# Kernel optimization log

Measured on AMD Instinct MI355X. Metric: run time of the kernel, lower is better.

## Reference

```python
import jax, jax.numpy as jnp
import numpy as np

NUM_LAYERS, E, H = 4, 256, 8
HD = E // H
EPS = 1e-5


def _layer_norm(x, g, b):
    m = jnp.mean(x, axis=-1, keepdims=True)
    v = jnp.mean((x - m) ** 2, axis=-1, keepdims=True)
    return (x - m) / jnp.sqrt(v + EPS) * g + b


def _embed_rotary(x, pos):
    # x: [B, L, E], pos: [B, L, E, 2] (cos, sin)
    x2 = jnp.stack([-x[..., 1::2], x[..., ::2]], axis=-1).reshape(x.shape)
    return x * pos[..., 0] + x2 * pos[..., 1]


def setup_inputs() -> dict:
    key = jax.random.key(0)
    ks = jax.random.split(key, 16)
    Lq, B, Lkv = 512, 4, 4096
    s = 0.02
    return {
        "query": jax.random.normal(ks[0], (Lq, B, E), jnp.float32),
        "value": jax.random.normal(ks[1], (Lkv, B, E), jnp.float32),
        "query_pos": jax.random.normal(ks[2], (B, Lq, E, 2), jnp.float32),
        "value_pos": jax.random.normal(ks[3], (B, Lkv, E, 2), jnp.float32),
        "Wqkv": jax.random.normal(ks[4], (NUM_LAYERS, 3 * E, E), jnp.float32) * s,
        "bqkv": jnp.zeros((NUM_LAYERS, 3 * E), jnp.float32),
        "Wo": jax.random.normal(ks[5], (NUM_LAYERS, E, E), jnp.float32) * s,
        "bo": jnp.zeros((NUM_LAYERS, E), jnp.float32),
        "ln1_g": jnp.ones((NUM_LAYERS, E), jnp.float32),
        "ln1_b": jnp.zeros((NUM_LAYERS, E), jnp.float32),
        "W1": jax.random.normal(ks[6], (NUM_LAYERS, E, E), jnp.float32) * s,
        "b1": jnp.zeros((NUM_LAYERS, E), jnp.float32),
        "W2": jax.random.normal(ks[7], (NUM_LAYERS, E, E), jnp.float32) * s,
        "b2": jnp.zeros((NUM_LAYERS, E), jnp.float32),
        "ln2_g": jnp.ones((NUM_LAYERS, E), jnp.float32),
        "ln2_b": jnp.zeros((NUM_LAYERS, E), jnp.float32),
    }


def reference(query, value, query_pos, value_pos, Wqkv, bqkv, Wo, bo,
              ln1_g, ln1_b, W1, b1, W2, b2, ln2_g, ln2_b):
    Lq, B, _ = query.shape
    Lkv = value.shape[0]
    scale = HD ** -0.5

    def step(q_in, p):
        Wqkv_l, bqkv_l, Wo_l, bo_l, g1, be1, W1_l, b1_l, W2_l, b2_l, g2, be2 = p
        Wq, Wk, Wv = jnp.split(Wqkv_l, 3, axis=0)
        bq, bk, bv = jnp.split(bqkv_l, 3, axis=0)
        q = (q_in @ Wq.T + bq) * scale              # [Lq, B, E] (scaled as torch MHA)
        k = value @ Wk.T + bk                        # [Lkv, B, E]
        v = value @ Wv.T + bv
        qb = _embed_rotary(q.swapaxes(0, 1), query_pos)   # [B, Lq, E]
        kb = _embed_rotary(k.swapaxes(0, 1), value_pos)   # [B, Lkv, E]
        vb = v.swapaxes(0, 1)
        qh = qb.reshape(B, Lq, H, HD).transpose(0, 2, 1, 3)    # [B, H, Lq, HD]
        kh = kb.reshape(B, Lkv, H, HD).transpose(0, 2, 1, 3)
        vh = vb.reshape(B, Lkv, H, HD).transpose(0, 2, 1, 3)
        attn = jax.nn.softmax(jnp.einsum('bhqd,bhkd->bhqk', qh, kh), axis=-1)
        o = jnp.einsum('bhqk,bhkd->bhqd', attn, vh)            # [B, H, Lq, HD]
        o = o.transpose(0, 2, 1, 3).reshape(B, Lq, E).swapaxes(0, 1)  # [Lq, B, E]
        x = _layer_norm(q_in + o @ Wo_l.T + bo_l, g1, be1)
        ff = jax.nn.relu(x @ W1_l.T + b1_l) @ W2_l.T + b2_l
        y = _layer_norm(x + ff, g2, be2)
        return y, y

    params = (Wqkv, bqkv, Wo, bo, ln1_g, ln1_b, W1, b1, W2, b2, ln2_g, ln2_b)
    _, ys = jax.lax.scan(step, query, params)
    return ys  # [num_layers, Lq, B, E] — stacked per-layer outputs
```

## Files before the change

### kernel.cpp

```cpp
#include <hip/hip_runtime.h>
#include <hip/hip_bf16.h>

typedef __attribute__((ext_vector_type(8))) short short8;
typedef __attribute__((ext_vector_type(4))) float float4v;

#define LQ 512
#define NB 4
#define LKV 4096
#define E 256
#define NH 8
#define HD 32
#define NLAYER 4
#define QSCALE 0.17677669529663687f
#define SPLITS 8
#define KSPAN (LKV / SPLITS)
#define QT 128
#define CK 128

#define LDS_FENCE() asm volatile("s_waitcnt lgkmcnt(0)" ::: "memory")

__device__ __forceinline__ unsigned short f2bf(float f) {
    union { float f; unsigned int i; } x; x.f = f;
    unsigned int r = x.i + 0x7fffu + ((x.i >> 16) & 1u);
    return (unsigned short)(r >> 16);
}
__device__ __forceinline__ unsigned int pack2(float a, float b) {
    union { float f; unsigned int i; } xa, xb; xa.f = a; xb.f = b;
    unsigned int ra = xa.i + 0x7fffu + ((xa.i >> 16) & 1u);
    unsigned int rb = xb.i + 0x7fffu + ((xb.i >> 16) & 1u);
    return (ra >> 16) | (rb & 0xffff0000u);
}
__device__ __forceinline__ unsigned int pack2_rtz(float a, float b) {
    union { float f; unsigned int i; } xa, xb; xa.f = a; xb.f = b;
    return __builtin_amdgcn_perm(xb.i, xa.i, 0x07060302u);
}
__device__ __forceinline__ float bf2f(unsigned short u) {
    union { unsigned int i; float f; } x; x.i = ((unsigned int)u) << 16; return x.f;
}
__device__ __forceinline__ float4v mfma16(short8 a, short8 b, float4v c) {
    return __builtin_amdgcn_mfma_f32_16x16x32_bf16(a, b, c, 0, 0, 0);
}
__device__ __forceinline__ void pack_store8(const float* __restrict__ src,
                                            unsigned short* __restrict__ dst) {
    float4 a = *(const float4*)src;
    float4 b = *(const float4*)(src + 4);
    uint4 v;
    v.x = pack2(a.x, a.y); v.y = pack2(a.z, a.w);
    v.z = pack2(b.x, b.y); v.w = pack2(b.z, b.w);
    *(uint4*)dst = v;
}

__global__ void pack_all(const float* __restrict__ value, const float* __restrict__ Wqkv,
                         const float* __restrict__ Wo, const float* __restrict__ W1,
                         const float* __restrict__ W2, const float* __restrict__ qpos,
                         const float* __restrict__ vpos, const float* __restrict__ query,
                         unsigned short* __restrict__ val_t, unsigned short* __restrict__ wqkv_bf,
                         unsigned short* __restrict__ wo_bf, unsigned short* __restrict__ w1_bf,
                         unsigned short* __restrict__ w2_bf, unsigned short* __restrict__ qpos_bf,
                         unsigned short* __restrict__ vpos_bf, float* __restrict__ cur,
                         unsigned short* __restrict__ cur_bf) {
    int bid = blockIdx.x;
    if (bid < 2048) {
        long idx = ((long)bid * 256 + threadIdx.x) * 8;
        int ro = (int)(idx >> 8), e = (int)(idx & 255);
        int ri = ((ro & 4095) << 2) | (ro >> 12);
        pack_store8(value + (long)ri * 256 + e, val_t + idx);
        return;
    }
    bid -= 2048;
    if (bid < 384) { long i = ((long)bid * 256 + threadIdx.x) * 8; pack_store8(Wqkv + i, wqkv_bf + i); return; }
    bid -= 384;
    if (bid < 128) { long i = ((long)bid * 256 + threadIdx.x) * 8; pack_store8(Wo + i, wo_bf + i); return; }
    bid -= 128;
    if (bid < 128) { long i = ((long)bid * 256 + threadIdx.x) * 8; pack_store8(W1 + i, w1_bf + i); return; }
    bid -= 128;
    if (bid < 128) { long i = ((long)bid * 256 + threadIdx.x) * 8; pack_store8(W2 + i, w2_bf + i); return; }
    bid -= 128;
    if (bid < 512) { long i = ((long)bid * 256 + threadIdx.x) * 8; pack_store8(qpos + i, qpos_bf + i); return; }
    bid -= 512;
    if (bid < 4096) { long i = ((long)bid * 256 + threadIdx.x) * 8; pack_store8(vpos + i, vpos_bf + i); return; }
    bid -= 4096;
    {
        long i = ((long)bid * 256 + threadIdx.x) * 8;
        float4 a = *(const float4*)&query[i];
        float4 b = *(const float4*)&query[i + 4];
        *(float4*)&cur[i] = a;
        *(float4*)&cur[i + 4] = b;
        uint4 v;
        v.x = pack2(a.x, a.y); v.y = pack2(a.z, a.w);
        v.z = pack2(b.x, b.y); v.w = pack2(b.z, b.w);
        *(uint4*)&cur_bf[i] = v;
    }
}

__global__ __launch_bounds__(256) void gemm_k(
        const unsigned short* __restrict__ A, const unsigned short* __restrict__ W,
        const float* __restrict__ bias, unsigned short* __restrict__ out_bf) {
    __shared__ unsigned short sA[32 * 264];
    __shared__ unsigned short sB[64 * 264];
    const int t = threadIdx.x;
    const int lane = t & 63, wave = t >> 6, quad = lane >> 4, lid = lane & 15;
    const int row0 = blockIdx.x * 32, col0 = blockIdx.y * 64;
    {
        int r = t >> 3, ks = (t & 7) * 32;
        const unsigned short* ap = A + (long)(row0 + r) * E + ks;
#pragma unroll
        for (int i = 0; i < 4; i++)
            *(uint4*)&sA[r * 264 + ks + i * 8] = *(const uint4*)(ap + i * 8);
    }
    {
        int r = t >> 2, ks = (t & 3) * 64;
        const unsigned short* wp = W + (long)(col0 + r) * E + ks;
#pragma unroll
        for (int i = 0; i < 8; i++)
            *(uint4*)&sB[r * 264 + ks + i * 8] = *(const uint4*)(wp + i * 8);
    }
    __syncthreads();
    float4v acc[2];
    acc[0] = (float4v){0.f, 0.f, 0.f, 0.f};
    acc[1] = (float4v){0.f, 0.f, 0.f, 0.f};
#pragma unroll
    for (int k0 = 0; k0 < E; k0 += 32) {
        short8 bf = *(const short8*)&sB[(wave * 16 + lid) * 264 + k0 + quad * 8];
        short8 af0 = *(const short8*)&sA[(lid) * 264 + k0 + quad * 8];
        short8 af1 = *(const short8*)&sA[(16 + lid) * 264 + k0 + quad * 8];
        acc[0] = mfma16(af0, bf, acc[0]);
        acc[1] = mfma16(af1, bf, acc[1]);
    }
#pragma unroll
    for (int mt = 0; mt < 2; mt++)
#pragma unroll
        for (int r = 0; r < 4; r++) {
            int grow = row0 + mt * 16 + quad * 4 + r;
            int gcol = col0 + wave * 16 + lid;
            float v = fmaxf(acc[mt][r] + bias[gcol], 0.f);
            out_bf[(long)grow * E + gcol] = f2bf(v);
        }
}

template <int COMBINE, int OUT2>
__global__ __launch_bounds__(256, 1) void gemm_ln(
        const unsigned short* __restrict__ A,
        const float* __restrict__ Opart, const float* __restrict__ lp,
        const unsigned short* __restrict__ W, const float* __restrict__ bias,
        const float* __restrict__ res, const float* __restrict__ g,
        const float* __restrict__ bvec, float* __restrict__ outf,
        unsigned short* __restrict__ out_bf, float* __restrict__ outf2) {
    __shared__ unsigned short sA[16 * 264];
    __shared__ float lnS[4][16];
    __shared__ float lnQ[4][16];
    const int t = threadIdx.x;
    const int lane = t & 63, wave = t >> 6, quad = lane >> 4, lid = lane & 15;
    const int row0 = blockIdx.x * 16;
    {
        const int r = t >> 4, cseg = t & 15;
        if (COMBINE) {
            const int grow = row0 + r;
            const int seq = grow >> 2, b = grow & 3;
            const int h = cseg >> 1, dd = (cseg & 1) * 16;
            const int bh = b * 8 + h;
            float L = 0.f;
            float av[16];
#pragma unroll
            for (int j = 0; j < 16; j++) av[j] = 0.f;
#pragma unroll
            for (int s = 0; s < SPLITS; s++) {
                long rbase = (long)(s * 32 + bh) * 512 + seq;
                L += lp[rbase];
#pragma unroll
                for (int jj = 0; jj < 4; jj++) {
                    float4 p = *(const float4*)&Opart[rbase * 32 + dd + jj * 4];
                    av[jj * 4 + 0] += p.x; av[jj * 4 + 1] += p.y;
                    av[jj * 4 + 2] += p.z; av[jj * 4 + 3] += p.w;
                }
            }
            float inv = 1.f / L;
            uint4 u0, u1;
            u0.x = pack2(av[0] * inv, av[1] * inv);   u0.y = pack2(av[2] * inv, av[3] * inv);
            u0.z = pack2(av[4] * inv, av[5] * inv);   u0.w = pack2(av[6] * inv, av[7] * inv);
            u1.x = pack2(av[8] * inv, av[9] * inv);   u1.y = pack2(av[10] * inv, av[11] * inv);
            u1.z = pack2(av[12] * inv, av[13] * inv); u1.w = pack2(av[14] * inv, av[15] * inv);
            *(uint4*)&sA[r * 264 + cseg * 16] = u0;
            *(uint4*)&sA[r * 264 + cseg * 16 + 8] = u1;
        } else {
            const unsigned short* ap = A + (long)(row0 + r) * E + cseg * 16;
            *(uint4*)&sA[r * 264 + cseg * 16] = *(const uint4*)ap;
            *(uint4*)&sA[r * 264 + cseg * 16 + 8] = *(const uint4*)(ap + 8);
        }
    }
    __syncthreads();
    float4v acc[4];
#pragma unroll
    for (int nf = 0; nf < 4; nf++) acc[nf] = (float4v){0.f, 0.f, 0.f, 0.f};
#pragma unroll
    for (int k0 = 0; k0 < E; k0 += 32) {
        short8 af = *(const short8*)&sA[lid * 264 + k0 + quad * 8];
#pragma unroll
        for (int nf = 0; nf < 4; nf++) {
            short8 bf = *(const short8*)(W + (long)(wave * 64 + nf * 16 + lid) * E + k0 + quad * 8);
            acc[nf] = mfma16(af, bf, acc[nf]);
        }
    }
    float v[4][4];
    float sr[4], qr_[4];
#pragma unroll
    for (int r = 0; r < 4; r++) { sr[r] = 0.f; qr_[r] = 0.f; }
#pragma unroll
    for (int nf = 0; nf < 4; nf++) {
        int col = wave * 64 + nf * 16 + lid;
        float bcol = bias[col];
#pragma unroll
        for (int r = 0; r < 4; r++) {
            int grow = row0 + quad * 4 + r;
            float val = acc[nf][r] + bcol + res[(long)grow * E + col];
            v[nf][r] = val;
            sr[r] += val;
            qr_[r] += val * val;
        }
    }
#pragma unroll
    for (int r = 0; r < 4; r++) {
#pragma unroll
        for (int d = 1; d < 16; d <<= 1) {
            sr[r] += __shfl_xor(sr[r], d);
            qr_[r] += __shfl_xor(qr_[r], d);
        }
    }
    if (lid == 0) {
#pragma unroll
        for (int r = 0; r < 4; r++) {
            lnS[wave][quad * 4 + r] = sr[r];
            lnQ[wave][quad * 4 + r] = qr_[r];
        }
    }
    __syncthreads();
    float mean[4], rstd[4];
#pragma unroll
    for (int r = 0; r < 4; r++) {
        int row = quad * 4 + r;
        float S = lnS[0][row] + lnS[1][row] + lnS[2][row] + lnS[3][row];
        float Q = lnQ[0][row] + lnQ[1][row] + lnQ[2][row] + lnQ[3][row];
        float mu = S * (1.f / 256.f);
        float var = Q * (1.f / 256.f) - mu * mu;
        mean[r] = mu;
        rstd[r] = rsqrtf(var + 1e-5f);
    }
#pragma unroll
    for (int nf = 0; nf < 4; nf++) {
        int col = wave * 64 + nf * 16 + lid;
        float gc = g[col], bc = bvec[col];
#pragma unroll
        for (int r = 0; r < 4; r++) {
            int grow = row0 + quad * 4 + r;
            float xo = (v[nf][r] - mean[r]) * rstd[r] * gc + bc;
            outf[(long)grow * E + col] = xo;
            out_bf[(long)grow * E + col] = f2bf(xo);
            if (OUT2) outf2[(long)grow * E + col] = xo;
        }
    }
}

__global__ __launch_bounds__(256) void qkv_q(
        const unsigned short* __restrict__ A, const unsigned short* __restrict__ W,
        const float* __restrict__ bias, const unsigned short* __restrict__ pos,
        unsigned short* __restrict__ qout) {
    __shared__ unsigned short sA[32 * 40];
    __shared__ unsigned short sB[64 * 40];
    const int t = threadIdx.x;
    const int lane = t & 63, wave = t >> 6, quad = lane >> 4, lid = lane & 15;
    const int row0 = blockIdx.x * 32, col0 = blockIdx.y * 64;
    const int sr = t >> 2, sk = (t & 3) * 8;
    const unsigned short* ap = A + (long)(row0 + sr) * E + sk;
    const unsigned short* wp = W + (long)(col0 + sr) * E + sk;
    uint4 av, bv;
    if (t < 128) av = *(const uint4*)ap;
    bv = *(const uint4*)wp;
    float4v acc[2];
    acc[0] = (float4v){0.f, 0.f, 0.f, 0.f};
    acc[1] = (float4v){0.f, 0.f, 0.f, 0.f};
#pragma unroll
    for (int ki = 0; ki < 8; ki++) {
        __syncthreads();
        if (t < 128) *(uint4*)&sA[sr * 40 + sk] = av;
        *(uint4*)&sB[sr * 40 + sk] = bv;
        __syncthreads();
        if (ki < 7) {
            if (t < 128) av = *(const uint4*)(ap + (ki + 1) * 32);
            bv = *(const uint4*)(wp + (ki + 1) * 32);
        }
        short8 af0 = *(const short8*)&sA[lid * 40 + quad * 8];
        short8 af1 = *(const short8*)&sA[(16 + lid) * 40 + quad * 8];
        short8 bf = *(const short8*)&sB[(wave * 16 + lid) * 40 + quad * 8];
        acc[0] = mfma16(af0, bf, acc[0]);
        acc[1] = mfma16(af1, bf, acc[1]);
    }
#pragma unroll
    for (int mt = 0; mt < 2; mt++)
#pragma unroll
        for (int r = 0; r < 4; r++) {
            int grow = row0 + mt * 16 + quad * 4 + r;
            int gcol = col0 + wave * 16 + lid;
            float v = (acc[mt][r] + bias[gcol]) * QSCALE;
            int seq = grow >> 2, b = grow & 3;
            int c = gcol;
            unsigned int cs = *(const unsigned int*)&pos[(((long)b * LQ + seq) * E + c) * 2];
            float cv = bf2f((unsigned short)cs), sv = bf2f((unsigned short)(cs >> 16));
            float p = __shfl_xor(v, 1);
            float x2 = (c & 1) ? p : -p;
            float rv = v * cv + x2 * sv;
            qout[(((long)b * NH + (c >> 5)) * LQ + seq) * HD + (c & 31)] = f2bf(rv);
        }
}

__global__ __launch_bounds__(256) void qkv_kv(
        const unsigned short* __restrict__ A, const unsigned short* __restrict__ Wall,
        const float* __restrict__ ball, const unsigned short* __restrict__ pos,
        unsigned short* __restrict__ kall, unsigned short* __restrict__ vtall) {
    const int layer = blockIdx.z;
    const unsigned short* W = Wall + (long)layer * 768 * 256 + 256 * 256;
    const float* bias = ball + (long)layer * 768 + 256;
    unsigned short* kout = kall + (long)layer * 4194304;
    unsigned short* vtout = vtall + (long)layer * 4194304;
    __shared__ unsigned short sA[64 * 72];
    __shared__ unsigned short sB[64 * 72];
    __shared__ unsigned short sT[64 * 72];
    const int t = threadIdx.x;
    const int lane = t & 63, wave = t >> 6, quad = lane >> 4, lid = lane & 15;
    const int wr = wave >> 1, wc = wave & 1;
    const int row0 = blockIdx.x * 64, col0 = blockIdx.y * 64;
    const int b = row0 >> 12, seq0 = row0 & 4095;
    const int r = t >> 2, kk = (t & 3) * 16;
    const unsigned short* apg = A + (long)(row0 + r) * E + kk;
    const unsigned short* wpg = W + (long)(col0 + r) * E + kk;
    uint4 a0 = *(const uint4*)apg,        a1 = *(const uint4*)(apg + 8);
    uint4 b0 = *(const uint4*)wpg,        b1 = *(const uint4*)(wpg + 8);
    float4v acc[2][2];
    for (int i = 0; i < 2; i++) for (int j = 0; j < 2; j++) acc[i][j] = (float4v){0.f, 0.f, 0.f, 0.f};
#pragma unroll
    for (int ki = 0; ki < 4; ki++) {
        __syncthreads();
        *(uint4*)&sA[r * 72 + kk] = a0; *(uint4*)&sA[r * 72 + kk + 8] = a1;
        *(uint4*)&sB[r * 72 + kk] = b0; *(uint4*)&sB[r * 72 + kk + 8] = b1;
        __syncthreads();
        if (ki < 3) {
            a0 = *(const uint4*)(apg + (ki + 1) * 64); a1 = *(const uint4*)(apg + (ki + 1) * 64 + 8);
            b0 = *(const uint4*)(wpg + (ki + 1) * 64); b1 = *(const uint4*)(wpg + (ki + 1) * 64 + 8);
        }
#pragma unroll
        for (int kf = 0; kf < 2; kf++) {
            const int ko = kf * 32 + quad * 8;
            short8 af0 = *(const short8*)&sA[(wr * 32 + lid) * 72 + ko];
            short8 af1 = *(const short8*)&sA[(wr * 32 + 16 + lid) * 72 + ko];
            short8 bf0 = *(const short8*)&sB[(wc * 32 + lid) * 72 + ko];
            short8 bf1 = *(const short8*)&sB[(wc * 32 + 16 + lid) * 72 + ko];
            acc[0][0] = mfma16(af0, bf0, acc[0][0]);
            acc[0][1] = mfma16(af0, bf1, acc[0][1]);
            acc[1][0] = mfma16(af1, bf0, acc[1][0]);
            acc[1][1] = mfma16(af1, bf1, acc[1][1]);
        }
    }
    if (col0 < 256) {
#pragma unroll
        for (int mt = 0; mt < 2; mt++)
#pragma unroll
            for (int nt = 0; nt < 2; nt++)
#pragma unroll
                for (int rr = 0; rr < 4; rr++) {
                    int m = wr * 32 + mt * 16 + quad * 4 + rr;
                    int c = col0 + wc * 32 + nt * 16 + lid;
                    int seq = seq0 + m;
                    float v = acc[mt][nt][rr] + bias[c];
                    unsigned int cs = *(const unsigned int*)&pos[(((long)b * LKV + seq) * E + c) * 2];
                    float cv = bf2f((unsigned short)cs), sv = bf2f((unsigned short)(cs >> 16));
                    float p = __shfl_xor(v, 1);
                    float x2 = (c & 1) ? p : -p;
                    float rv = v * cv + x2 * sv;
                    kout[(((long)b * NH + (c >> 5)) * LKV + seq) * HD + (c & 31)] = f2bf(rv);
                }
    } else {
#pragma unroll
        for (int mt = 0; mt < 2; mt++)
#pragma unroll
            for (int nt = 0; nt < 2; nt++) {
                int cl = wc * 32 + nt * 16 + lid;
                int so = wr * 32 + mt * 16 + quad * 4;
                float bcol = bias[col0 + cl];
                uint2 pw;
                pw.x = pack2(acc[mt][nt][0] + bcol, acc[mt][nt][1] + bcol);
                pw.y = pack2(acc[mt][nt][2] + bcol, acc[mt][nt][3] + bcol);
                *(uint2*)&sT[cl * 72 + so] = pw;
            }
        __syncthreads();
        const int cl = t >> 2, sc = (t & 3) * 16;
        uint4 u0 = *(const uint4*)&sT[cl * 72 + sc];
        uint4 u1 = *(const uint4*)&sT[cl * 72 + sc + 8];
        int cg = (col0 - 256) + cl;
        unsigned short* dst = vtout + (((long)b * NH + (cg >> 5)) * HD + (cg & 31)) * (long)LKV + seq0 + sc;
        *(uint4*)dst = u0;
        *(uint4*)(dst + 8) = u1;
    }
}

__global__ __launch_bounds__(256) void attn_k(
        const unsigned short* __restrict__ qb, const unsigned short* __restrict__ kb,
        const unsigned short* __restrict__ vtb, float* __restrict__ Opart,
        float* __restrict__ lpart) {
    __shared__ unsigned short sK[CK * 40];
    __shared__ unsigned short sVT[32 * 136];
    __shared__ unsigned short sPT[4 * 64 * 36];
    const int t = threadIdx.x;
    const int lane = t & 63, wave = t >> 6, quad = lane >> 4, lid = lane & 15;
    const int qt0 = blockIdx.x * QT;
    const int bh = blockIdx.y;
    const int key0 = blockIdx.z * KSPAN;
    const unsigned short* kbase = kb + (long)bh * LKV * HD;
    const unsigned short* vbase = vtb + (long)bh * HD * LKV;
    short8 aq[2];
#pragma unroll
    for (int mf = 0; mf < 2; mf++)
        aq[mf] = *(const short8*)(qb + ((long)bh * LQ + qt0 + wave * 32 + mf * 16 + lid) * HD + quad * 8);
    float4v o[2][2];
#pragma unroll
    for (int i = 0; i < 2; i++) for (int j = 0; j < 2; j++) o[i][j] = (float4v){0.f, 0.f, 0.f, 0.f};
    float l[8] = {0.f, 0.f, 0.f, 0.f, 0.f, 0.f, 0.f, 0.f};
    const int krow = t >> 1, khalf = (t & 1) * 16;
    const int vrow = t >> 3, vkoff = (t & 7) * 16;
    unsigned short* myPT = &sPT[wave * 64 * 36];
    uint4 kv0 = *(const uint4*)(kbase + (long)(key0 + krow) * HD + khalf);
    uint4 kv1 = *(const uint4*)(kbase + (long)(key0 + krow) * HD + khalf + 8);
    uint4 vv0 = *(const uint4*)(vbase + (long)vrow * LKV + key0 + vkoff);
    uint4 vv1 = *(const uint4*)(vbase + (long)vrow * LKV + key0 + vkoff + 8);
    for (int ck = key0; ck < key0 + KSPAN; ck += CK) {
        __syncthreads();
        *(uint4*)&sK[krow * 40 + khalf] = kv0;
        *(uint4*)&sK[krow * 40 + khalf + 8] = kv1;
        *(uint4*)&sVT[vrow * 136 + vkoff] = vv0;
        *(uint4*)&sVT[vrow * 136 + vkoff + 8] = vv1;
        __syncthreads();
        if (ck + CK < key0 + KSPAN) {
            kv0 = *(const uint4*)(kbase + (long)(ck + CK + krow) * HD + khalf);
            kv1 = *(const uint4*)(kbase + (long)(ck + CK + krow) * HD + khalf + 8);
            vv0 = *(const uint4*)(vbase + (long)vrow * LKV + ck + CK + vkoff);
            vv1 = *(const uint4*)(vbase + (long)vrow * LKV + ck + CK + vkoff + 8);
        }
#pragma unroll
        for (int half = 0; half < 2; half++) {
#pragma unroll
            for (int nf = 0; nf < 4; nf++) {
                short8 bk = *(const short8*)&sK[(half * 64 + nf * 16 + lid) * 40 + quad * 8];
#pragma unroll
                for (int mf = 0; mf < 2; mf++) {
                    float4v z = (float4v){0.f, 0.f, 0.f, 0.f};
                    float4v s = mfma16(aq[mf], bk, z);
                    float e0 = __expf(s[0]), e1 = __expf(s[1]);
                    float e2 = __expf(s[2]), e3 = __expf(s[3]);
                    l[mf * 4 + 0] += e0; l[mf * 4 + 1] += e1;
                    l[mf * 4 + 2] += e2; l[mf * 4 + 3] += e3;
                    uint2 pk;
                    pk.x = pack2_rtz(e0, e1);
                    pk.y = pack2_rtz(e2, e3);
                    *(uint2*)&myPT[(nf * 16 + lid) * 36 + mf * 16 + quad * 4] = pk;
                }
            }
            LDS_FENCE();
#pragma unroll
            for (int kb2 = 0; kb2 < 2; kb2++) {
                short8 bv0 = *(const short8*)&sVT[lid * 136 + half * 64 + kb2 * 32 + quad * 8];
                short8 bv1 = *(const short8*)&sVT[(16 + lid) * 136 + half * 64 + kb2 * 32 + quad * 8];
#pragma unroll
                for (int mf = 0; mf < 2; mf++) {
                    short8 ap;
#pragma unroll
                    for (int j = 0; j < 8; j++)
                        ap[j] = (short)myPT[(kb2 * 32 + quad * 8 + j) * 36 + mf * 16 + lid];
                    o[mf][0] = mfma16(ap, bv0, o[mf][0]);
                    o[mf][1] = mfma16(ap, bv1, o[mf][1]);
                }
            }
            LDS_FENCE();
        }
    }
#pragma unroll
    for (int i = 0; i < 8; i++) {
#pragma unroll
        for (int d = 1; d < 16; d <<= 1) l[i] += __shfl_xor(l[i], d);
    }
#pragma unroll
    for (int mf = 0; mf < 2; mf++)
#pragma unroll
        for (int r = 0; r < 4; r++) {
            long orow = ((long)blockIdx.z * 32 + bh) * LQ + qt0 + wave * 32 + mf * 16 + quad * 4 + r;
            Opart[orow * HD + lid] = o[mf][0][r];
            Opart[orow * HD + 16 + lid] = o[mf][1][r];
            if (lid == 0) lpart[orow] = l[mf * 4 + r];
        }
}

extern "C" void kernel_launch(void* const* d_in, const int* in_sizes, int n_in,
                              void* d_out, int out_size, void* d_ws, size_t ws_size,
                              hipStream_t stream) {
    (void)in_sizes; (void)n_in; (void)out_size; (void)ws_size;
    const float* query = (const float*)d_in[0];
    const float* value = (const float*)d_in[1];
    const float* qpos  = (const float*)d_in[2];
    const float* vpos  = (const float*)d_in[3];
    const float* Wqkv  = (const float*)d_in[4];
    const float* bqkv  = (const float*)d_in[5];
    const float* Wo    = (const float*)d_in[6];
    const float* bo    = (const float*)d_in[7];
    const float* g1    = (const float*)d_in[8];
    const float* be1   = (const float*)d_in[9];
    const float* W1    = (const float*)d_in[10];
    const float* b1    = (const float*)d_in[11];
    const float* W2    = (const float*)d_in[12];
    const float* b2    = (const float*)d_in[13];
    const float* g2    = (const float*)d_in[14];
    const float* be2   = (const float*)d_in[15];
    float* outp = (float*)d_out;

    char* w = (char*)d_ws;
    float*          cur     = (float*)(w + 0);
    unsigned short* cur_bf  = (unsigned short*)(w + (2l  << 20));
    unsigned short* qbuf    = (unsigned short*)(w + (3l  << 20));
    float*          xb      = (float*)(w + (4l  << 20));
    unsigned short* xb_bf   = (unsigned short*)(w + (6l  << 20));
    unsigned short* h1b_bf  = (unsigned short*)(w + (7l  << 20));
    float*          lp      = (float*)(w + (8l  << 20));
    float*          Opart   = (float*)(w + (9l  << 20));
    unsigned short* val_t   = (unsigned short*)(w + (25l << 20));
    unsigned short* wqkv_bf = (unsigned short*)(w + (33l << 20));
    unsigned short* wo_bf   = (unsigned short*)(w + (35l << 20));
    unsigned short* w1_bf   = (unsigned short*)(w + (36l << 20));
    unsigned short* w2_bf   = (unsigned short*)(w + (37l << 20));
    unsigned short* qpos_bf = (unsigned short*)(w + (38l << 20));
    unsigned short* vpos_bf = (unsigned short*)(w + (40l << 20));
    unsigned short* kbuf    = (unsigned short*)(w + (56l << 20));
    unsigned short* vtb     = (unsigned short*)(w + (88l << 20));

    pack_all<<<7680, 256, 0, stream>>>(value, Wqkv, Wo, W1, W2, qpos, vpos, query,
                                       val_t, wqkv_bf, wo_bf, w1_bf, w2_bf, qpos_bf,
                                       vpos_bf, cur, cur_bf);

    qkv_kv<<<dim3(256, 8, NLAYER), 256, 0, stream>>>(val_t, wqkv_bf, bqkv, vpos_bf, kbuf, vtb);

    for (int layer = 0; layer < NLAYER; layer++) {
        const unsigned short* Wl = wqkv_bf + (long)layer * 768 * 256;
        const float* bl = bqkv + (long)layer * 768;
        qkv_q<<<dim3(64, 4), 256, 0, stream>>>(cur_bf, Wl, bl, qpos_bf, qbuf);
        attn_k<<<dim3(LQ / QT, 32, SPLITS), 256, 0, stream>>>(
            qbuf, kbuf + (long)layer * 4194304, vtb + (long)layer * 4194304, Opart, lp);
        gemm_ln<1, 0><<<128, 256, 0, stream>>>(
            nullptr, Opart, lp, wo_bf + layer * 65536, bo + layer * 256,
            cur, g1 + layer * 256, be1 + layer * 256, xb, xb_bf, nullptr);
        gemm_k<<<dim3(64, 4), 256, 0, stream>>>(xb_bf, w1_bf + layer * 65536, b1 + layer * 256, h1b_bf);
        gemm_ln<0, 1><<<128, 256, 0, stream>>>(
            h1b_bf, nullptr, nullptr, w2_bf + layer * 65536, b2 + layer * 256,
            xb, g2 + layer * 256, be2 + layer * 256, cur, cur_bf,
            outp + (long)layer * LQ * NB * E);
    }
}
```

Baseline: 379.4 us.

## Keep attention probabilities in registers via shuffles and fuse FFN into one kernel

The attention kernel now computes S transposed (K as the A operand), so exponentiated scores can be rearranged into the PV MFMA operand layout with cross-lane shuffles. This removes the LDS round-trip and fences for the P tile, and the row-sum reduction shrinks to two xor shuffles. The FFN's two GEMMs are fused into one kernel that keeps the ReLU hidden activations in LDS, which drops one launch per layer and the global h1 buffer. The qkv_kv kernel also reuses one LDS region for the transpose buffer, lowering its shared memory use. In exchange, the FFN kernel runs only 128 blocks, each doing both GEMMs serially, and attention adds many shuffle instructions.

```diff
diff --git a/kernel.cpp b/kernel.cpp
--- a/kernel.cpp
+++ b/kernel.cpp
@@ -16,8 +16,6 @@
 #define KSPAN (LKV / SPLITS)
 #define QT 128
 #define CK 128
-
-#define LDS_FENCE() asm volatile("s_waitcnt lgkmcnt(0)" ::: "memory")
 
 __device__ __forceinline__ unsigned short f2bf(float f) {
     union { float f; unsigned int i; } x; x.f = f;
@@ -93,59 +91,12 @@
     }
 }
 
-__global__ __launch_bounds__(256) void gemm_k(
-        const unsigned short* __restrict__ A, const unsigned short* __restrict__ W,
-        const float* __restrict__ bias, unsigned short* __restrict__ out_bf) {
-    __shared__ unsigned short sA[32 * 264];
-    __shared__ unsigned short sB[64 * 264];
-    const int t = threadIdx.x;
-    const int lane = t & 63, wave = t >> 6, quad = lane >> 4, lid = lane & 15;
-    const int row0 = blockIdx.x * 32, col0 = blockIdx.y * 64;
-    {
-        int r = t >> 3, ks = (t & 7) * 32;
-        const unsigned short* ap = A + (long)(row0 + r) * E + ks;
-#pragma unroll
-        for (int i = 0; i < 4; i++)
-            *(uint4*)&sA[r * 264 + ks + i * 8] = *(const uint4*)(ap + i * 8);
-    }
-    {
-        int r = t >> 2, ks = (t & 3) * 64;
-        const unsigned short* wp = W + (long)(col0 + r) * E + ks;
-#pragma unroll
-        for (int i = 0; i < 8; i++)
-            *(uint4*)&sB[r * 264 + ks + i * 8] = *(const uint4*)(wp + i * 8);
-    }
-    __syncthreads();
-    float4v acc[2];
-    acc[0] = (float4v){0.f, 0.f, 0.f, 0.f};
-    acc[1] = (float4v){0.f, 0.f, 0.f, 0.f};
-#pragma unroll
-    for (int k0 = 0; k0 < E; k0 += 32) {
-        short8 bf = *(const short8*)&sB[(wave * 16 + lid) * 264 + k0 + quad * 8];
-        short8 af0 = *(const short8*)&sA[(lid) * 264 + k0 + quad * 8];
-        short8 af1 = *(const short8*)&sA[(16 + lid) * 264 + k0 + quad * 8];
-        acc[0] = mfma16(af0, bf, acc[0]);
-        acc[1] = mfma16(af1, bf, acc[1]);
-    }
-#pragma unroll
-    for (int mt = 0; mt < 2; mt++)
-#pragma unroll
-        for (int r = 0; r < 4; r++) {
-            int grow = row0 + mt * 16 + quad * 4 + r;
-            int gcol = col0 + wave * 16 + lid;
-            float v = fmaxf(acc[mt][r] + bias[gcol], 0.f);
-            out_bf[(long)grow * E + gcol] = f2bf(v);
-        }
-}
-
-template <int COMBINE, int OUT2>
-__global__ __launch_bounds__(256, 1) void gemm_ln(
-        const unsigned short* __restrict__ A,
+__global__ __launch_bounds__(256, 1) void wo_ln(
         const float* __restrict__ Opart, const float* __restrict__ lp,
         const unsigned short* __restrict__ W, const float* __restrict__ bias,
         const float* __restrict__ res, const float* __restrict__ g,
         const float* __restrict__ bvec, float* __restrict__ outf,
-        unsigned short* __restrict__ out_bf, float* __restrict__ outf2) {
+        unsigned short* __restrict__ out_bf) {
     __shared__ unsigned short sA[16 * 264];
     __shared__ float lnS[4][16];
     __shared__ float lnQ[4][16];
@@ -154,39 +105,33 @@
     const int row0 = blockIdx.x * 16;
     {
         const int r = t >> 4, cseg = t & 15;
-        if (COMBINE) {
-            const int grow = row0 + r;
-            const int seq = grow >> 2, b = grow & 3;
-            const int h = cseg >> 1, dd = (cseg & 1) * 16;
-            const int bh = b * 8 + h;
-            float L = 0.f;
-            float av[16];
-#pragma unroll
-            for (int j = 0; j < 16; j++) av[j] = 0.f;
-#pragma unroll
-            for (int s = 0; s < SPLITS; s++) {
-                long rbase = (long)(s * 32 + bh) * 512 + seq;
-                L += lp[rbase];
-#pragma unroll
-                for (int jj = 0; jj < 4; jj++) {
-                    float4 p = *(const float4*)&Opart[rbase * 32 + dd + jj * 4];
-                    av[jj * 4 + 0] += p.x; av[jj * 4 + 1] += p.y;
-                    av[jj * 4 + 2] += p.z; av[jj * 4 + 3] += p.w;
-                }
+        const int grow = row0 + r;
+        const int seq = grow >> 2, b = grow & 3;
+        const int h = cseg >> 1, dd = (cseg & 1) * 16;
+        const int bh = b * 8 + h;
+        float L = 0.f;
+        float av[16];
+#pragma unroll
+        for (int j = 0; j < 16; j++) av[j] = 0.f;
+#pragma unroll
+        for (int s = 0; s < SPLITS; s++) {
+            long rbase = (long)(s * 32 + bh) * 512 + seq;
+            L += lp[rbase];
+#pragma unroll
+            for (int jj = 0; jj < 4; jj++) {
+                float4 p = *(const float4*)&Opart[rbase * 32 + dd + jj * 4];
+                av[jj * 4 + 0] += p.x; av[jj * 4 + 1] += p.y;
+                av[jj * 4 + 2] += p.z; av[jj * 4 + 3] += p.w;
             }
-            float inv = 1.f / L;
-            uint4 u0, u1;
-            u0.x = pack2(av[0] * inv, av[1] * inv);   u0.y = pack2(av[2] * inv, av[3] * inv);
-            u0.z = pack2(av[4] * inv, av[5] * inv);   u0.w = pack2(av[6] * inv, av[7] * inv);
-            u1.x = pack2(av[8] * inv, av[9] * inv);   u1.y = pack2(av[10] * inv, av[11] * inv);
-            u1.z = pack2(av[12] * inv, av[13] * inv); u1.w = pack2(av[14] * inv, av[15] * inv);
-            *(uint4*)&sA[r * 264 + cseg * 16] = u0;
-            *(uint4*)&sA[r * 264 + cseg * 16 + 8] = u1;
-        } else {
-            const unsigned short* ap = A + (long)(row0 + r) * E + cseg * 16;
-            *(uint4*)&sA[r * 264 + cseg * 16] = *(const uint4*)ap;
-            *(uint4*)&sA[r * 264 + cseg * 16 + 8] = *(const uint4*)(ap + 8);
-        }
+        }
+        float inv = 1.f / L;
+        uint4 u0, u1;
+        u0.x = pack2(av[0] * inv, av[1] * inv);   u0.y = pack2(av[2] * inv, av[3] * inv);
+        u0.z = pack2(av[4] * inv, av[5] * inv);   u0.w = pack2(av[6] * inv, av[7] * inv);
+        u1.x = pack2(av[8] * inv, av[9] * inv);   u1.y = pack2(av[10] * inv, av[11] * inv);
+        u1.z = pack2(av[12] * inv, av[13] * inv); u1.w = pack2(av[14] * inv, av[15] * inv);
+        *(uint4*)&sA[r * 264 + cseg * 16] = u0;
+        *(uint4*)&sA[r * 264 + cseg * 16 + 8] = u1;
     }
     __syncthreads();
     float4v acc[4];
@@ -241,9 +186,8 @@
         float S = lnS[0][row] + lnS[1][row] + lnS[2][row] + lnS[3][row];
         float Q = lnQ[0][row] + lnQ[1][row] + lnQ[2][row] + lnQ[3][row];
         float mu = S * (1.f / 256.f);
-        float var = Q * (1.f / 256.f) - mu * mu;
         mean[r] = mu;
-        rstd[r] = rsqrtf(var + 1e-5f);
+        rstd[r] = rsqrtf(Q * (1.f / 256.f) - mu * mu + 1e-5f);
     }
 #pragma unroll
     for (int nf = 0; nf < 4; nf++) {
@@ -255,7 +199,117 @@
             float xo = (v[nf][r] - mean[r]) * rstd[r] * gc + bc;
             outf[(long)grow * E + col] = xo;
             out_bf[(long)grow * E + col] = f2bf(xo);
-            if (OUT2) outf2[(long)grow * E + col] = xo;
+        }
+    }
+}
+
+__global__ __launch_bounds__(256, 1) void ffn_ln(
+        const unsigned short* __restrict__ A, const unsigned short* __restrict__ W1,
+        const float* __restrict__ b1, const unsigned short* __restrict__ W2,
+        const float* __restrict__ b2, const float* __restrict__ res,
+        const float* __restrict__ g, const float* __restrict__ bvec,
+        float* __restrict__ outf, unsigned short* __restrict__ out_bf,
+        float* __restrict__ outf2) {
+    __shared__ unsigned short sA[16 * 264];
+    __shared__ unsigned short sH[16 * 264];
+    __shared__ float lnS[4][16];
+    __shared__ float lnQ[4][16];
+    const int t = threadIdx.x;
+    const int lane = t & 63, wave = t >> 6, quad = lane >> 4, lid = lane & 15;
+    const int row0 = blockIdx.x * 16;
+    {
+        const int r = t >> 4, cseg = t & 15;
+        const unsigned short* ap = A + (long)(row0 + r) * E + cseg * 16;
+        *(uint4*)&sA[r * 264 + cseg * 16] = *(const uint4*)ap;
+        *(uint4*)&sA[r * 264 + cseg * 16 + 8] = *(const uint4*)(ap + 8);
+    }
+    __syncthreads();
+    float4v acc[4];
+#pragma unroll
+    for (int nf = 0; nf < 4; nf++) acc[nf] = (float4v){0.f, 0.f, 0.f, 0.f};
+#pragma unroll
+    for (int k0 = 0; k0 < E; k0 += 32) {
+        short8 af = *(const short8*)&sA[lid * 264 + k0 + quad * 8];
+#pragma unroll
+        for (int nf = 0; nf < 4; nf++) {
+            short8 bf = *(const short8*)(W1 + (long)(wave * 64 + nf * 16 + lid) * E + k0 + quad * 8);
+            acc[nf] = mfma16(af, bf, acc[nf]);
+        }
+    }
+#pragma unroll
+    for (int nf = 0; nf < 4; nf++) {
+        int col = wave * 64 + nf * 16 + lid;
+        float bc = b1[col];
+#pragma unroll
+        for (int r = 0; r < 4; r++)
+            sH[(quad * 4 + r) * 264 + col] = f2bf(fmaxf(acc[nf][r] + bc, 0.f));
+    }
+    __syncthreads();
+#pragma unroll
+    for (int nf = 0; nf < 4; nf++) acc[nf] = (float4v){0.f, 0.f, 0.f, 0.f};
+#pragma unroll
+    for (int k0 = 0; k0 < E; k0 += 32) {
+        short8 af = *(const short8*)&sH[lid * 264 + k0 + quad * 8];
+#pragma unroll
+        for (int nf = 0; nf < 4; nf++) {
+            short8 bf = *(const short8*)(W2 + (long)(wave * 64 + nf * 16 + lid) * E + k0 + quad * 8);
+            acc[nf] = mfma16(af, bf, acc[nf]);
+        }
+    }
+    float v[4][4];
+    float sr[4], qr_[4];
+#pragma unroll
+    for (int r = 0; r < 4; r++) { sr[r] = 0.f; qr_[r] = 0.f; }
+#pragma unroll
+    for (int nf = 0; nf < 4; nf++) {
+        int col = wave * 64 + nf * 16 + lid;
+        float bcol = b2[col];
+#pragma unroll
+        for (int r = 0; r < 4; r++) {
+            int grow = row0 + quad * 4 + r;
+            float val = acc[nf][r] + bcol + res[(long)grow * E + col];
+            v[nf][r] = val;
+            sr[r] += val;
+            qr_[r] += val * val;
+        }
+    }
+#pragma unroll
+    for (int r = 0; r < 4; r++) {
+#pragma unroll
+        for (int d = 1; d < 16; d <<= 1) {
+            sr[r] += __shfl_xor(sr[r], d);
+            qr_[r] += __shfl_xor(qr_[r], d);
+        }
+    }
+    if (lid == 0) {
+#pragma unroll
+        for (int r = 0; r < 4; r++) {
+            lnS[wave][quad * 4 + r] = sr[r];
+            lnQ[wave][quad * 4 + r] = qr_[r];
+        }
+    }
+    __syncthreads();
+    float mean[4], rstd[4];
+#pragma unroll
+    for (int r = 0; r < 4; r++) {
+        int row = quad * 4 + r;
+        float S = lnS[0][row] + lnS[1][row] + lnS[2][row] + lnS[3][row];
+        float Q = lnQ[0][row] + lnQ[1][row] + lnQ[2][row] + lnQ[3][row];
+        float mu = S * (1.f / 256.f);
+        mean[r] = mu;
+        rstd[r] = rsqrtf(Q * (1.f / 256.f) - mu * mu + 1e-5f);
+    }
+#pragma unroll
+    for (int nf = 0; nf < 4; nf++) {
+        int col = wave * 64 + nf * 16 + lid;
+        float gc = g[col], bc = bvec[col];
+#pragma unroll
+        for (int r = 0; r < 4; r++) {
+            int grow = row0 + quad * 4 + r;
+            float xo = (v[nf][r] - mean[r]) * rstd[r] * gc + bc;
+            outf[(long)grow * E + col] = xo;
+            out_bf[(long)grow * E + col] = f2bf(xo);
+            outf2[(long)grow * E + col] = xo;
         }
     }
 }
@@ -321,9 +375,9 @@
     const float* bias = ball + (long)layer * 768 + 256;
     unsigned short* kout = kall + (long)layer * 4194304;
     unsigned short* vtout = vtall + (long)layer * 4194304;
-    __shared__ unsigned short sA[64 * 72];
-    __shared__ unsigned short sB[64 * 72];
-    __shared__ unsigned short sT[64 * 72];
+    __shared__ unsigned short smem[2 * 64 * 72];
+    unsigned short* sA = smem;
+    unsigned short* sB = smem + 64 * 72;
     const int t = threadIdx.x;
     const int lane = t & 63, wave = t >> 6, quad = lane >> 4, lid = lane & 15;
     const int wr = wave >> 1, wc = wave & 1;
@@ -378,6 +432,8 @@
                     kout[(((long)b * NH + (c >> 5)) * LKV + seq) * HD + (c & 31)] = f2bf(rv);
                 }
     } else {
+        __syncthreads();
+        unsigned short* sT = smem;
 #pragma unroll
         for (int mt = 0; mt < 2; mt++)
 #pragma unroll
@@ -407,7 +463,6 @@
         float* __restrict__ lpart) {
     __shared__ unsigned short sK[CK * 40];
     __shared__ unsigned short sVT[32 * 136];
-    __shared__ unsigned short sPT[4 * 64 * 36];
     const int t = threadIdx.x;
     const int lane = t & 63, wave = t >> 6, quad = lane >> 4, lid = lane & 15;
     const int qt0 = blockIdx.x * QT;
@@ -422,10 +477,11 @@
     float4v o[2][2];
 #pragma unroll
     for (int i = 0; i < 2; i++) for (int j = 0; j < 2; j++) o[i][j] = (float4v){0.f, 0.f, 0.f, 0.f};
-    float l[8] = {0.f, 0.f, 0.f, 0.f, 0.f, 0.f, 0.f, 0.f};
+    float lq[2] = {0.f, 0.f};
     const int krow = t >> 1, khalf = (t & 1) * 16;
     const int vrow = t >> 3, vkoff = (t & 7) * 16;
-    unsigned short* myPT = &sPT[wave * 64 * 36];
+    const int L0 = (quad & 1) * 32 + lid, L1 = L0 + 16;
+    const bool hi = quad >= 2;
     uint4 kv0 = *(const uint4*)(kbase + (long)(key0 + krow) * HD + khalf);
     uint4 kv1 = *(const uint4*)(kbase + (long)(key0 + krow) * HD + khalf + 8);
     uint4 vv0 = *(const uint4*)(vbase + (long)vrow * LKV + key0 + vkoff);
@@ -444,56 +500,55 @@
             vv1 = *(const uint4*)(vbase + (long)vrow * LKV + ck + CK + vkoff + 8);
         }
 #pragma unroll
-        for (int half = 0; half < 2; half++) {
-#pragma unroll
-            for (int nf = 0; nf < 4; nf++) {
-                short8 bk = *(const short8*)&sK[(half * 64 + nf * 16 + lid) * 40 + quad * 8];
-#pragma unroll
-                for (int mf = 0; mf < 2; mf++) {
-                    float4v z = (float4v){0.f, 0.f, 0.f, 0.f};
-                    float4v s = mfma16(aq[mf], bk, z);
-                    float e0 = __expf(s[0]), e1 = __expf(s[1]);
-                    float e2 = __expf(s[2]), e3 = __expf(s[3]);
-                    l[mf * 4 + 0] += e0; l[mf * 4 + 1] += e1;
-                    l[mf * 4 + 2] += e2; l[mf * 4 + 3] += e3;
-                    uint2 pk;
-                    pk.x = pack2_rtz(e0, e1);
-                    pk.y = pack2_rtz(e2, e3);
-                    *(uint2*)&myPT[(nf * 16 + lid) * 36 + mf * 16 + quad * 4] = pk;
-                }
+        for (int sub = 0; sub < 4; sub++) {
+            short8 bk0 = *(const short8*)&sK[(sub * 32 + lid) * 40 + quad * 8];
+            short8 bk1 = *(const short8*)&sK[(sub * 32 + 16 + lid) * 40 + quad * 8];
+            short8 bv0 = *(const short8*)&sVT[lid * 136 + sub * 32 + quad * 8];
+            short8 bv1 = *(const short8*)&sVT[(16 + lid) * 136 + sub * 32 + quad * 8];
+#pragma unroll
+            for (int mf = 0; mf < 2; mf++) {
+                float4v z = (float4v){0.f, 0.f, 0.f, 0.f};
+                float4v f0 = mfma16(bk0, aq[mf], z);
+                float4v f1 = mfma16(bk1, aq[mf], z);
+                float e0 = __expf(f0[0]), e1 = __expf(f0[1]);
+                float e2 = __expf(f0[2]), e3 = __expf(f0[3]);
+                float g0 = __expf(f1[0]), g1 = __expf(f1[1]);
+                float g2 = __expf(f1[2]), g3 = __expf(f1[3]);
+                lq[mf] += ((e0 + e1) + (e2 + e3)) + ((g0 + g1) + (g2 + g3));
+                unsigned int pA01 = pack2_rtz(e0, e1), pA23 = pack2_rtz(e2, e3);
+                unsigned int pB01 = pack2_rtz(g0, g1), pB23 = pack2_rtz(g2, g3);
+                unsigned int a01_0 = __shfl((int)pA01, L0), a23_0 = __shfl((int)pA23, L0);
+                unsigned int b01_0 = __shfl((int)pB01, L0), b23_0 = __shfl((int)pB23, L0);
+                unsigned int a01_1 = __shfl((int)pA01, L1), a23_1 = __shfl((int)pA23, L1);
+                unsigned int b01_1 = __shfl((int)pB01, L1), b23_1 = __shfl((int)pB23, L1);
+                union { unsigned int u[4]; short8 s; } ap;
+                ap.u[0] = hi ? b01_0 : a01_0;
+                ap.u[1] = hi ? b23_0 : a23_0;
+                ap.u[2] = hi ? b01_1 : a01_1;
+                ap.u[3] = hi ? b23_1 : a23_1;
+                o[mf][0] = mfma16(ap.s, bv0, o[mf][0]);
+                o[mf][1] = mfma16(ap.s, bv1, o[mf][1]);
             }
-            LDS_FENCE();
-#pragma unroll
-            for (int kb2 = 0; kb2 < 2; kb2++) {
-                short8 bv0 = *(const short8*)&sVT[lid * 136 + half * 64 + kb2 * 32 + quad * 8];
-                short8 bv1 = *(const short8*)&sVT[(16 + lid) * 136 + half * 64 + kb2 * 32 + quad * 8];
-#pragma unroll
-                for (int mf = 0; mf < 2; mf++) {
-                    short8 ap;
-#pragma unroll
-                    for (int j = 0; j < 8; j++)
-                        ap[j] = (short)myPT[(kb2 * 32 + quad * 8 + j) * 36 + mf * 16 + lid];
-                    o[mf][0] = mfma16(ap, bv0, o[mf][0]);
-                    o[mf][1] = mfma16(ap, bv1, o[mf][1]);
-                }
-            }
-            LDS_FENCE();
-        }
-    }
-#pragma unroll
-    for (int i = 0; i < 8; i++) {
-#pragma unroll
-        for (int d = 1; d < 16; d <<= 1) l[i] += __shfl_xor(l[i], d);
-    }
-#pragma unroll
-    for (int mf = 0; mf < 2; mf++)
+        }
+    }
+#pragma unroll
+    for (int mf = 0; mf < 2; mf++) {
+        lq[mf] += __shfl_xor(lq[mf], 16);
+        lq[mf] += __shfl_xor(lq[mf], 32);
+    }
+#pragma unroll
+    for (int mf = 0; mf < 2; mf++) {
 #pragma unroll
         for (int r = 0; r < 4; r++) {
             long orow = ((long)blockIdx.z * 32 + bh) * LQ + qt0 + wave * 32 + mf * 16 + quad * 4 + r;
             Opart[orow * HD + lid] = o[mf][0][r];
             Opart[orow * HD + 16 + lid] = o[mf][1][r];
-            if (lid == 0) lpart[orow] = l[mf * 4 + r];
-        }
+        }
+        if (quad == 0) {
+            long orow = ((long)blockIdx.z * 32 + bh) * LQ + qt0 + wave * 32 + mf * 16 + lid;
+            lpart[orow] = lq[mf];
+        }
+    }
 }
 
 extern "C" void kernel_launch(void* const* d_in, const int* in_sizes, int n_in,
@@ -524,7 +579,6 @@
     unsigned short* qbuf    = (unsigned short*)(w + (3l  << 20));
     float*          xb      = (float*)(w + (4l  << 20));
     unsigned short* xb_bf   = (unsigned short*)(w + (6l  << 20));
-    unsigned short* h1b_bf  = (unsigned short*)(w + (7l  << 20));
     float*          lp      = (float*)(w + (8l  << 20));
     float*          Opart   = (float*)(w + (9l  << 20));
     unsigned short* val_t   = (unsigned short*)(w + (25l << 20));
@@ -549,12 +603,12 @@
         qkv_q<<<dim3(64, 4), 256, 0, stream>>>(cur_bf, Wl, bl, qpos_bf, qbuf);
         attn_k<<<dim3(LQ / QT, 32, SPLITS), 256, 0, stream>>>(
             qbuf, kbuf + (long)layer * 4194304, vtb + (long)layer * 4194304, Opart, lp);
-        gemm_ln<1, 0><<<128, 256, 0, stream>>>(
-            nullptr, Opart, lp, wo_bf + layer * 65536, bo + layer * 256,
-            cur, g1 + layer * 256, be1 + layer * 256, xb, xb_bf, nullptr);
-        gemm_k<<<dim3(64, 4), 256, 0, stream>>>(xb_bf, w1_bf + layer * 65536, b1 + layer * 256, h1b_bf);
-        gemm_ln<0, 1><<<128, 256, 0, stream>>>(
-            h1b_bf, nullptr, nullptr, w2_bf + layer * 65536, b2 + layer * 256,
+        wo_ln<<<128, 256, 0, stream>>>(
+            Opart, lp, wo_bf + layer * 65536, bo + layer * 256,
+            cur, g1 + layer * 256, be1 + layer * 256, xb, xb_bf);
+        ffn_ln<<<128, 256, 0, stream>>>(
+            xb_bf, w1_bf + layer * 65536, b1 + layer * 256,
+            w2_bf + layer * 65536, b2 + layer * 256,
             xb, g2 + layer * 256, be2 + layer * 256, cur, cur_bf,
             outp + (long)layer * LQ * NB * E);
     }
```

Result: slower. 397.5 us (+4.8%).

## Loop layers inside K/V projection kernel, reusing staged activations and rotary tables

Applied to the files above, without the earlier changes.

The K/V projection kernel now loads its 64x256 activation tile into shared memory once, along with the rotary cos/sin values, and then loops over all four layers inside one block. It no longer launches one grid slice per layer that reloads the same data. Weight fragments are read straight from global memory instead of being staged through shared memory. This removes redundant activation and position loads and cuts per-tile synchronisation. In exchange the grid is four times smaller, so fewer blocks are in flight, and weight reads become uncoalesced per-lane global loads.

```diff
diff --git a/kernel.cpp b/kernel.cpp
--- a/kernel.cpp
+++ b/kernel.cpp
@@ -241,9 +241,8 @@
         float S = lnS[0][row] + lnS[1][row] + lnS[2][row] + lnS[3][row];
         float Q = lnQ[0][row] + lnQ[1][row] + lnQ[2][row] + lnQ[3][row];
         float mu = S * (1.f / 256.f);
-        float var = Q * (1.f / 256.f) - mu * mu;
         mean[r] = mu;
-        rstd[r] = rsqrtf(var + 1e-5f);
+        rstd[r] = rsqrtf(Q * (1.f / 256.f) - mu * mu + 1e-5f);
     }
 #pragma unroll
     for (int nf = 0; nf < 4; nf++) {
@@ -316,88 +315,99 @@
         const unsigned short* __restrict__ A, const unsigned short* __restrict__ Wall,
         const float* __restrict__ ball, const unsigned short* __restrict__ pos,
         unsigned short* __restrict__ kall, unsigned short* __restrict__ vtall) {
-    const int layer = blockIdx.z;
-    const unsigned short* W = Wall + (long)layer * 768 * 256 + 256 * 256;
-    const float* bias = ball + (long)layer * 768 + 256;
-    unsigned short* kout = kall + (long)layer * 4194304;
-    unsigned short* vtout = vtall + (long)layer * 4194304;
-    __shared__ unsigned short sA[64 * 72];
-    __shared__ unsigned short sB[64 * 72];
+    __shared__ unsigned short sA[64 * 264];
     __shared__ unsigned short sT[64 * 72];
     const int t = threadIdx.x;
     const int lane = t & 63, wave = t >> 6, quad = lane >> 4, lid = lane & 15;
     const int wr = wave >> 1, wc = wave & 1;
     const int row0 = blockIdx.x * 64, col0 = blockIdx.y * 64;
     const int b = row0 >> 12, seq0 = row0 & 4095;
-    const int r = t >> 2, kk = (t & 3) * 16;
-    const unsigned short* apg = A + (long)(row0 + r) * E + kk;
-    const unsigned short* wpg = W + (long)(col0 + r) * E + kk;
-    uint4 a0 = *(const uint4*)apg,        a1 = *(const uint4*)(apg + 8);
-    uint4 b0 = *(const uint4*)wpg,        b1 = *(const uint4*)(wpg + 8);
-    float4v acc[2][2];
-    for (int i = 0; i < 2; i++) for (int j = 0; j < 2; j++) acc[i][j] = (float4v){0.f, 0.f, 0.f, 0.f};
-#pragma unroll
-    for (int ki = 0; ki < 4; ki++) {
-        __syncthreads();
-        *(uint4*)&sA[r * 72 + kk] = a0; *(uint4*)&sA[r * 72 + kk + 8] = a1;
-        *(uint4*)&sB[r * 72 + kk] = b0; *(uint4*)&sB[r * 72 + kk + 8] = b1;
-        __syncthreads();
-        if (ki < 3) {
-            a0 = *(const uint4*)(apg + (ki + 1) * 64); a1 = *(const uint4*)(apg + (ki + 1) * 64 + 8);
-            b0 = *(const uint4*)(wpg + (ki + 1) * 64); b1 = *(const uint4*)(wpg + (ki + 1) * 64 + 8);
-        }
-#pragma unroll
-        for (int kf = 0; kf < 2; kf++) {
-            const int ko = kf * 32 + quad * 8;
-            short8 af0 = *(const short8*)&sA[(wr * 32 + lid) * 72 + ko];
-            short8 af1 = *(const short8*)&sA[(wr * 32 + 16 + lid) * 72 + ko];
-            short8 bf0 = *(const short8*)&sB[(wc * 32 + lid) * 72 + ko];
-            short8 bf1 = *(const short8*)&sB[(wc * 32 + 16 + lid) * 72 + ko];
+    const bool khalf_blk = (col0 < 256);
+    {
+        const int r = t >> 2, kk = (t & 3) * 64;
+        const unsigned short* ap = A + (long)(row0 + r) * E + kk;
+#pragma unroll
+        for (int i = 0; i < 8; i++)
+            *(uint4*)&sA[r * 264 + kk + i * 8] = *(const uint4*)(ap + i * 8);
+    }
+    unsigned int cs[2][2][4];
+    if (khalf_blk) {
+#pragma unroll
+        for (int mt = 0; mt < 2; mt++)
+#pragma unroll
+            for (int nt = 0; nt < 2; nt++)
+#pragma unroll
+                for (int rr = 0; rr < 4; rr++) {
+                    int seq = seq0 + wr * 32 + mt * 16 + quad * 4 + rr;
+                    int c = col0 + wc * 32 + nt * 16 + lid;
+                    cs[mt][nt][rr] = *(const unsigned int*)&pos[(((long)b * LKV + seq) * E + c) * 2];
+                }
+    }
+    __syncthreads();
+    const unsigned short* wb0base = Wall + 256 * 256 + (long)(col0 + wc * 32 + lid) * E;
+    const unsigned short* wb1base = Wall + 256 * 256 + (long)(col0 + wc * 32 + 16 + lid) * E;
+    for (int layer = 0; layer < NLAYER; layer++) {
+        const float* bias = ball + (long)layer * 768 + 256;
+        const unsigned short* wb0 = wb0base + (long)layer * 768 * 256;
+        const unsigned short* wb1 = wb1base + (long)layer * 768 * 256;
+        float4v acc[2][2];
+#pragma unroll
+        for (int i = 0; i < 2; i++)
+#pragma unroll
+            for (int j = 0; j < 2; j++) acc[i][j] = (float4v){0.f, 0.f, 0.f, 0.f};
+#pragma unroll
+        for (int k0 = 0; k0 < E; k0 += 32) {
+            short8 bf0 = *(const short8*)(wb0 + k0 + quad * 8);
+            short8 bf1 = *(const short8*)(wb1 + k0 + quad * 8);
+            short8 af0 = *(const short8*)&sA[(wr * 32 + lid) * 264 + k0 + quad * 8];
+            short8 af1 = *(const short8*)&sA[(wr * 32 + 16 + lid) * 264 + k0 + quad * 8];
             acc[0][0] = mfma16(af0, bf0, acc[0][0]);
             acc[0][1] = mfma16(af0, bf1, acc[0][1]);
             acc[1][0] = mfma16(af1, bf0, acc[1][0]);
             acc[1][1] = mfma16(af1, bf1, acc[1][1]);
         }
-    }
-    if (col0 < 256) {
-#pragma unroll
-        for (int mt = 0; mt < 2; mt++)
-#pragma unroll
-            for (int nt = 0; nt < 2; nt++)
-#pragma unroll
-                for (int rr = 0; rr < 4; rr++) {
-                    int m = wr * 32 + mt * 16 + quad * 4 + rr;
-                    int c = col0 + wc * 32 + nt * 16 + lid;
-                    int seq = seq0 + m;
-                    float v = acc[mt][nt][rr] + bias[c];
-                    unsigned int cs = *(const unsigned int*)&pos[(((long)b * LKV + seq) * E + c) * 2];
-                    float cv = bf2f((unsigned short)cs), sv = bf2f((unsigned short)(cs >> 16));
-                    float p = __shfl_xor(v, 1);
-                    float x2 = (c & 1) ? p : -p;
-                    float rv = v * cv + x2 * sv;
-                    kout[(((long)b * NH + (c >> 5)) * LKV + seq) * HD + (c & 31)] = f2bf(rv);
+        if (khalf_blk) {
+            unsigned short* kout = kall + (long)layer * 4194304;
+#pragma unroll
+            for (int mt = 0; mt < 2; mt++)
+#pragma unroll
+                for (int nt = 0; nt < 2; nt++)
+#pragma unroll
+                    for (int rr = 0; rr < 4; rr++) {
+                        int c = col0 + wc * 32 + nt * 16 + lid;
+                        int seq = seq0 + wr * 32 + mt * 16 + quad * 4 + rr;
+                        float v = acc[mt][nt][rr] + bias[c];
+                        unsigned int u = cs[mt][nt][rr];
+                        float cv = bf2f((unsigned short)u), sv = bf2f((unsigned short)(u >> 16));
+                        float p = __shfl_xor(v, 1);
+                        float x2 = (c & 1) ? p : -p;
+                        float rv = v * cv + x2 * sv;
+                        kout[(((long)b * NH + (c >> 5)) * LKV + seq) * HD + (c & 31)] = f2bf(rv);
+                    }
+        } else {
+            unsigned short* vtout = vtall + (long)layer * 4194304;
+            __syncthreads();
+#pragma unroll
+            for (int mt = 0; mt < 2; mt++)
+#pragma unroll
+                for (int nt = 0; nt < 2; nt++) {
+                    int cl = wc * 32 + nt * 16 + lid;
+                    int so = wr * 32 + mt * 16 + quad * 4;
+                    float bcol = bias[col0 + cl];
+                    uint2 pw;
+                    pw.x = pack2(acc[mt][nt][0] + bcol, acc[mt][nt][1] + bcol);
+                    pw.y = pack2(acc[mt][nt][2] + bcol, acc[mt][nt][3] + bcol);
+                    *(uint2*)&sT[cl * 72 + so] = pw;
                 }
-    } else {
-#pragma unroll
-        for (int mt = 0; mt < 2; mt++)
-#pragma unroll
-            for (int nt = 0; nt < 2; nt++) {
-                int cl = wc * 32 + nt * 16 + lid;
-                int so = wr * 32 + mt * 16 + quad * 4;
-                float bcol = bias[col0 + cl];
-                uint2 pw;
-                pw.x = pack2(acc[mt][nt][0] + bcol, acc[mt][nt][1] + bcol);
-                pw.y = pack2(acc[mt][nt][2] + bcol, acc[mt][nt][3] + bcol);
-                *(uint2*)&sT[cl * 72 + so] = pw;
-            }
-        __syncthreads();
-        const int cl = t >> 2, sc = (t & 3) * 16;
-        uint4 u0 = *(const uint4*)&sT[cl * 72 + sc];
-        uint4 u1 = *(const uint4*)&sT[cl * 72 + sc + 8];
-        int cg = (col0 - 256) + cl;
-        unsigned short* dst = vtout + (((long)b * NH + (cg >> 5)) * HD + (cg & 31)) * (long)LKV + seq0 + sc;
-        *(uint4*)dst = u0;
-        *(uint4*)(dst + 8) = u1;
+            __syncthreads();
+            const int cl = t >> 2, sc = (t & 3) * 16;
+            uint4 u0 = *(const uint4*)&sT[cl * 72 + sc];
+            uint4 u1 = *(const uint4*)&sT[cl * 72 + sc + 8];
+            int cg = (col0 - 256) + cl;
+            unsigned short* dst = vtout + (((long)b * NH + (cg >> 5)) * HD + (cg & 31)) * (long)LKV + seq0 + sc;
+            *(uint4*)dst = u0;
+            *(uint4*)(dst + 8) = u1;
+        }
     }
 }
 
@@ -541,7 +551,7 @@
                                        val_t, wqkv_bf, wo_bf, w1_bf, w2_bf, qpos_bf,
                                        vpos_bf, cur, cur_bf);
 
-    qkv_kv<<<dim3(256, 8, NLAYER), 256, 0, stream>>>(val_t, wqkv_bf, bqkv, vpos_bf, kbuf, vtb);
+    qkv_kv<<<dim3(256, 8), 256, 0, stream>>>(val_t, wqkv_bf, bqkv, vpos_bf, kbuf, vtb);
 
     for (int layer = 0; layer < NLAYER; layer++) {
         const unsigned short* Wl = wqkv_bf + (long)layer * 768 * 256;
```

Result: slower. 422.5 us (+11.4%).
